# Optimization experiments

Measured on AMD Instinct MI355X. Metric: run time of the kernel, lower is better.

## Reference

```python
import jax, jax.numpy as jnp
import numpy as np

EPS = 1e-08
N = 8192
IN_F = 128
OUT_F = 128


def setup_inputs() -> dict:
    key = jax.random.key(0)
    k1, k2, k3, k4, k5 = jax.random.split(key, 5)
    x = jax.random.normal(k1, (N, IN_F), dtype=jnp.float32)
    adj = jax.random.uniform(k2, (N, N), dtype=jnp.float32)
    noise = jax.random.uniform(k3, (N, N), dtype=jnp.float32)
    # xavier_uniform bound = sqrt(6/(in+out))
    bound = float(np.sqrt(6.0 / (IN_F + OUT_F)))
    weight = jax.random.uniform(k4, (IN_F, OUT_F), dtype=jnp.float32,
                                minval=-bound, maxval=bound)
    learnable_adj = jax.random.uniform(k5, (N, N), dtype=jnp.float32)
    return {"x": x, "adj": adj, "noise": noise, "weight": weight,
            "learnable_adj": learnable_adj}


def reference(x, adj, noise, weight, learnable_adj):
    # noise_adj = adj + learnable_adj + eps * rand_like(adj)
    noise_adj = adj + learnable_adj + EPS * noise
    # add self loops (== + eye(N))
    n = noise_adj.shape[0]
    looped_adj = noise_adj + jnp.eye(n, dtype=noise_adj.dtype)
    # symmetric degree normalization: diag(d^-1/2) @ A @ diag(d^-1/2),
    # expressed as row/col broadcast scaling (same math, O(n^2))
    degree = jnp.sum(looped_adj, axis=1)              # (N,)
    d_inv_sqrt = (degree + EPS) ** -0.5               # (N,)
    normalized_adj = looped_adj * d_inv_sqrt[:, None] * d_inv_sqrt[None, :]
    support = x @ weight                              # (N, out)
    out = normalized_adj @ support                    # (N, out)
    return out
```

## Files before the change

### kernel.cpp

```cpp
#include <hip/hip_runtime.h>
#include <hip/hip_bf16.h>
#include <cstddef>

#define NN 8192
#define FF 128
#define EPSF 1e-8f
#define KSPLIT 8

typedef __attribute__((ext_vector_type(8))) short short8_t;
typedef __attribute__((ext_vector_type(4))) float f32x4_t;

static __device__ __forceinline__ unsigned short f2bf(float f) {
    unsigned u = __builtin_bit_cast(unsigned, f);
    u = (u + 0x7FFFu + ((u >> 16) & 1u)) >> 16;
    return (unsigned short)u;
}
static __device__ __forceinline__ float bf2f(unsigned short h) {
    return __builtin_bit_cast(float, ((unsigned)h) << 16);
}

__global__ __launch_bounds__(256) void fuse_combine_kernel(
    const float* __restrict__ adj, const float* __restrict__ learn,
    unsigned short* __restrict__ Lb, float* __restrict__ degree)
{
    const int row = blockIdx.x >> 1;
    const size_t base = (size_t)row * NN + (blockIdx.x & 1) * 4096
                      + (size_t)threadIdx.x * 8;
    const f32x4_t a0 = __builtin_nontemporal_load((const f32x4_t*)(adj + base));
    const f32x4_t a1 = __builtin_nontemporal_load((const f32x4_t*)(adj + base + 4));
    const f32x4_t a2 = __builtin_nontemporal_load((const f32x4_t*)(adj + base + 2048));
    const f32x4_t a3 = __builtin_nontemporal_load((const f32x4_t*)(adj + base + 2052));
    const f32x4_t l0 = __builtin_nontemporal_load((const f32x4_t*)(learn + base));
    const f32x4_t l1 = __builtin_nontemporal_load((const f32x4_t*)(learn + base + 4));
    const f32x4_t l2 = __builtin_nontemporal_load((const f32x4_t*)(learn + base + 2048));
    const f32x4_t l3 = __builtin_nontemporal_load((const f32x4_t*)(learn + base + 2052));

    const f32x4_t v0 = a0 + l0, v1 = a1 + l1, v2 = a2 + l2, v3 = a3 + l3;
    short8_t p0, p1;
    p0[0] = (short)f2bf(v0.x); p0[1] = (short)f2bf(v0.y);
    p0[2] = (short)f2bf(v0.z); p0[3] = (short)f2bf(v0.w);
    p0[4] = (short)f2bf(v1.x); p0[5] = (short)f2bf(v1.y);
    p0[6] = (short)f2bf(v1.z); p0[7] = (short)f2bf(v1.w);
    p1[0] = (short)f2bf(v2.x); p1[1] = (short)f2bf(v2.y);
    p1[2] = (short)f2bf(v2.z); p1[3] = (short)f2bf(v2.w);
    p1[4] = (short)f2bf(v3.x); p1[5] = (short)f2bf(v3.y);
    p1[6] = (short)f2bf(v3.z); p1[7] = (short)f2bf(v3.w);
    *(short8_t*)(Lb + base) = p0;
    *(short8_t*)(Lb + base + 2048) = p1;

    float acc = (v0.x + v0.y) + (v0.z + v0.w) + (v1.x + v1.y) + (v1.z + v1.w)
              + (v2.x + v2.y) + (v2.z + v2.w) + (v3.x + v3.y) + (v3.z + v3.w);
#pragma unroll
    for (int o = 32; o; o >>= 1) acc += __shfl_down(acc, o);
    __shared__ float red[4];
    if ((threadIdx.x & 63) == 0) red[threadIdx.x >> 6] = acc;
    __syncthreads();
    if (threadIdx.x == 0)
        atomicAdd(degree + row, red[0] + red[1] + red[2] + red[3]);
}

__global__ __launch_bounds__(256) void s_kernel(
    const float* __restrict__ degree, float* __restrict__ s)
{
    const int i = blockIdx.x * 256 + threadIdx.x;
    s[i] = rsqrtf(degree[i] + 1.0f + EPSF);
}

__global__ __launch_bounds__(256) void support_kernel(
    const float* __restrict__ x, const float* __restrict__ w,
    const float* __restrict__ s, unsigned short* __restrict__ ss_t)
{
    __shared__ float Ws[128 * 128];
    __shared__ float Xs[32][128];
    for (int i = threadIdx.x; i < 128 * 128 / 4; i += 256)
        ((float4*)Ws)[i] = ((const float4*)w)[i];
    const int rbase = blockIdx.x * 32;
    for (int i = threadIdx.x; i < 32 * 128 / 4; i += 256)
        ((float4*)&Xs[0][0])[i] = ((const float4*)(x + (size_t)rbase * 128))[i];
    __syncthreads();

    const int c = threadIdx.x & 127;
    const int h = threadIdx.x >> 7;
    for (int r = h; r < 32; r += 2) {
        float acc = 0.f;
#pragma unroll 8
        for (int k = 0; k < 128; ++k) acc += Xs[r][k] * Ws[k * 128 + c];
        const int grow = rbase + r;
        ss_t[(size_t)c * NN + grow] = f2bf(acc * s[grow]);
    }
}

template<bool ATOMIC>
__global__ __launch_bounds__(256) void spmm_bf16_kernel(
    const unsigned short* __restrict__ Lb,
    const unsigned short* __restrict__ ss_t,
    const float* __restrict__ s, float* __restrict__ outp)
{
    const int ks   = blockIdx.y;
    const int i0   = blockIdx.x * 128;
    const int wave = threadIdx.x >> 6;
    const int lane = threadIdx.x & 63;
    const int m = lane & 15;
    const int b = lane >> 4;
    const size_t a0off = (size_t)(i0 + wave * 32 + m) * NN;
    const size_t a1off = a0off + (size_t)16 * NN;
    const int kbeg = ks * (NN / KSPLIT);

    f32x4_t acc[2][8];
#pragma unroll
    for (int f = 0; f < 2; ++f)
#pragma unroll
        for (int t = 0; t < 8; ++t) acc[f][t] = (f32x4_t){0.f, 0.f, 0.f, 0.f};

    for (int kk = kbeg; kk < kbeg + NN / KSPLIT; kk += 32) {
        const int col = kk + 8 * b;
        const short8_t af0 = *(const short8_t*)(Lb + a0off + col);
        const short8_t af1 = *(const short8_t*)(Lb + a1off + col);
#pragma unroll
        for (int nt = 0; nt < 8; ++nt) {
            const short8_t bf =
                *(const short8_t*)(ss_t + (size_t)(nt * 16 + m) * NN + col);
            acc[0][nt] = __builtin_amdgcn_mfma_f32_16x16x32_bf16(af0, bf,
                                                                 acc[0][nt], 0, 0, 0);
            acc[1][nt] = __builtin_amdgcn_mfma_f32_16x16x32_bf16(af1, bf,
                                                                 acc[1][nt], 0, 0, 0);
        }
    }

#pragma unroll
    for (int f = 0; f < 2; ++f) {
#pragma unroll
        for (int nt = 0; nt < 8; ++nt) {
            const int n = nt * 16 + m;
#pragma unroll
            for (int r = 0; r < 4; ++r) {
                const int ro = i0 + wave * 32 + f * 16 + 4 * b + r;
                float v = acc[f][nt][r];
                if (ATOMIC) {
                    if (ks == 0) v += bf2f(ss_t[(size_t)n * NN + ro]);
                    atomicAdd(outp + (size_t)ro * FF + n, s[ro] * v);
                } else {
                    outp[(size_t)ks * NN * FF + (size_t)ro * FF + n] = v;
                }
            }
        }
    }
}

__global__ __launch_bounds__(256) void reduce_kernel(
    const float* __restrict__ part, const unsigned short* __restrict__ ss_t,
    const float* __restrict__ s, float* __restrict__ out)
{
    const int idx = blockIdx.x * 256 + threadIdx.x;
    const int gi = idx >> 7;
    const int cc = idx & 127;
    float v = 0.f;
#pragma unroll
    for (int k = 0; k < KSPLIT; ++k) v += part[(size_t)k * NN * FF + idx];
    v += bf2f(ss_t[(size_t)cc * NN + gi]);
    out[idx] = s[gi] * v;
}

extern "C" void kernel_launch(void* const* d_in, const int* in_sizes, int n_in,
                              void* d_out, int out_size, void* d_ws, size_t ws_size,
                              hipStream_t stream) {
    const float* x     = (const float*)d_in[0];
    const float* adj   = (const float*)d_in[1];
    const float* w     = (const float*)d_in[3];
    const float* learn = (const float*)d_in[4];
    float* out = (float*)d_out;

    float* degree = (float*)d_ws;
    float* s      = degree + NN;
    unsigned short* ss_t = (unsigned short*)(s + NN);
    unsigned short* Lb   = ss_t + (size_t)FF * NN;
    float* part          = (float*)(Lb + (size_t)NN * NN);

    const size_t need_base = 2 * NN * 4 + (size_t)FF * NN * 2
                           + (size_t)NN * NN * 2;
    const size_t need_part = need_base + (size_t)KSPLIT * NN * FF * 4;

    hipMemsetAsync(degree, 0, NN * sizeof(float), stream);
    fuse_combine_kernel<<<NN * 2, 256, 0, stream>>>(adj, learn, Lb, degree);
    s_kernel<<<NN / 256, 256, 0, stream>>>(degree, s);
    support_kernel<<<NN / 32, 256, 0, stream>>>(x, w, s, ss_t);

    if (ws_size >= need_part) {
        spmm_bf16_kernel<false><<<dim3(NN / 128, KSPLIT), 256, 0, stream>>>(
            Lb, ss_t, s, part);
        reduce_kernel<<<NN * FF / 256, 256, 0, stream>>>(part, ss_t, s, out);
    } else {
        hipMemsetAsync(d_out, 0, (size_t)NN * FF * sizeof(float), stream);
        spmm_bf16_kernel<true><<<dim3(NN / 128, KSPLIT), 256, 0, stream>>>(
            Lb, ss_t, s, out);
    }
}
```

Baseline: 258.1 us.

## Pre-swizzle bf16 adjacency and support into MFMA fragment-tiled layouts

The combine kernel now writes the bf16 adjacency in a blocked layout where each 16x32 MFMA A-fragment is contiguous, and the support kernel writes its transposed output in a matching B-fragment-tiled layout. The SpMM kernel then loads each fragment as one contiguous 1 KB chunk per wave instead of 16 rows strided by NN. This is meant to improve coalescing and cache-line use in the main GEMM, at the cost of scattered 16-byte stores in the producer kernels and more complex index math in the reduce epilogue.

Result: slower. 264.6 us (+2.5%).

```diff
diff --git a/kernel.cpp b/kernel.cpp
--- a/kernel.cpp
+++ b/kernel.cpp
@@ -19,13 +19,22 @@
     return __builtin_bit_cast(float, ((unsigned)h) << 16);
 }
 
+static __device__ __forceinline__ size_t lb2_idx(int row, int k) {
+    return ((size_t)(row >> 4) * 256 + (k >> 5)) * 512
+         + ((row & 15) * 4 + ((k >> 3) & 3)) * 8 + (k & 7);
+}
+static __device__ __forceinline__ size_t ss2_idx(int n, int k) {
+    return ((size_t)(k >> 5) * 8 + (n >> 4)) * 512
+         + ((n & 15) * 4 + ((k >> 3) & 3)) * 8 + (k & 7);
+}
+
 __global__ __launch_bounds__(256) void fuse_combine_kernel(
     const float* __restrict__ adj, const float* __restrict__ learn,
     unsigned short* __restrict__ Lb, float* __restrict__ degree)
 {
     const int row = blockIdx.x >> 1;
-    const size_t base = (size_t)row * NN + (blockIdx.x & 1) * 4096
-                      + (size_t)threadIdx.x * 8;
+    const int e0 = (blockIdx.x & 1) * 4096 + threadIdx.x * 8;
+    const size_t base = (size_t)row * NN + e0;
     const f32x4_t a0 = __builtin_nontemporal_load((const f32x4_t*)(adj + base));
     const f32x4_t a1 = __builtin_nontemporal_load((const f32x4_t*)(adj + base + 4));
     const f32x4_t a2 = __builtin_nontemporal_load((const f32x4_t*)(adj + base + 2048));
@@ -45,8 +54,8 @@
     p1[2] = (short)f2bf(v2.z); p1[3] = (short)f2bf(v2.w);
     p1[4] = (short)f2bf(v3.x); p1[5] = (short)f2bf(v3.y);
     p1[6] = (short)f2bf(v3.z); p1[7] = (short)f2bf(v3.w);
-    *(short8_t*)(Lb + base) = p0;
-    *(short8_t*)(Lb + base + 2048) = p1;
+    *(short8_t*)(Lb + lb2_idx(row, e0)) = p0;
+    *(short8_t*)(Lb + lb2_idx(row, e0 + 2048)) = p1;
 
     float acc = (v0.x + v0.y) + (v0.z + v0.w) + (v1.x + v1.y) + (v1.z + v1.w)
               + (v2.x + v2.y) + (v2.z + v2.w) + (v3.x + v3.y) + (v3.z + v3.w);
@@ -68,7 +77,7 @@
 
 __global__ __launch_bounds__(256) void support_kernel(
     const float* __restrict__ x, const float* __restrict__ w,
-    const float* __restrict__ s, unsigned short* __restrict__ ss_t)
+    const float* __restrict__ s, unsigned short* __restrict__ ss2)
 {
     __shared__ float Ws[128 * 128];
     __shared__ float Xs[32][128];
@@ -86,14 +95,14 @@
 #pragma unroll 8
         for (int k = 0; k < 128; ++k) acc += Xs[r][k] * Ws[k * 128 + c];
         const int grow = rbase + r;
-        ss_t[(size_t)c * NN + grow] = f2bf(acc * s[grow]);
+        ss2[ss2_idx(c, grow)] = f2bf(acc * s[grow]);
     }
 }
 
 template<bool ATOMIC>
 __global__ __launch_bounds__(256) void spmm_bf16_kernel(
     const unsigned short* __restrict__ Lb,
-    const unsigned short* __restrict__ ss_t,
+    const unsigned short* __restrict__ ss2,
     const float* __restrict__ s, float* __restrict__ outp)
 {
     const int ks   = blockIdx.y;
@@ -102,9 +111,9 @@
     const int lane = threadIdx.x & 63;
     const int m = lane & 15;
     const int b = lane >> 4;
-    const size_t a0off = (size_t)(i0 + wave * 32 + m) * NN;
-    const size_t a1off = a0off + (size_t)16 * NN;
-    const int kbeg = ks * (NN / KSPLIT);
+    const int laneoff = (m * 4 + b) * 8;
+    const int rb0 = (i0 >> 4) + wave * 2;
+    const int kb0 = ks * (256 / KSPLIT);
 
     f32x4_t acc[2][8];
 #pragma unroll
@@ -112,14 +121,17 @@
 #pragma unroll
         for (int t = 0; t < 8; ++t) acc[f][t] = (f32x4_t){0.f, 0.f, 0.f, 0.f};
 
-    for (int kk = kbeg; kk < kbeg + NN / KSPLIT; kk += 32) {
-        const int col = kk + 8 * b;
-        const short8_t af0 = *(const short8_t*)(Lb + a0off + col);
-        const short8_t af1 = *(const short8_t*)(Lb + a1off + col);
+    const unsigned short* a0p = Lb + (size_t)(rb0 + 0) * 256 * 512 + laneoff;
+    const unsigned short* a1p = Lb + (size_t)(rb0 + 1) * 256 * 512 + laneoff;
+    const unsigned short* bp  = ss2 + laneoff;
+
+    for (int kb = kb0; kb < kb0 + 256 / KSPLIT; ++kb) {
+        const short8_t af0 = *(const short8_t*)(a0p + (size_t)kb * 512);
+        const short8_t af1 = *(const short8_t*)(a1p + (size_t)kb * 512);
 #pragma unroll
         for (int nt = 0; nt < 8; ++nt) {
             const short8_t bf =
-                *(const short8_t*)(ss_t + (size_t)(nt * 16 + m) * NN + col);
+                *(const short8_t*)(bp + (size_t)kb * 4096 + nt * 512);
             acc[0][nt] = __builtin_amdgcn_mfma_f32_16x16x32_bf16(af0, bf,
                                                                  acc[0][nt], 0, 0, 0);
             acc[1][nt] = __builtin_amdgcn_mfma_f32_16x16x32_bf16(af1, bf,
@@ -137,7 +149,7 @@
                 const int ro = i0 + wave * 32 + f * 16 + 4 * b + r;
                 float v = acc[f][nt][r];
                 if (ATOMIC) {
-                    if (ks == 0) v += bf2f(ss_t[(size_t)n * NN + ro]);
+                    if (ks == 0) v += bf2f(ss2[ss2_idx(n, ro)]);
                     atomicAdd(outp + (size_t)ro * FF + n, s[ro] * v);
                 } else {
                     outp[(size_t)ks * NN * FF + (size_t)ro * FF + n] = v;
@@ -148,7 +160,7 @@
 }
 
 __global__ __launch_bounds__(256) void reduce_kernel(
-    const float* __restrict__ part, const unsigned short* __restrict__ ss_t,
+    const float* __restrict__ part, const unsigned short* __restrict__ ss2,
     const float* __restrict__ s, float* __restrict__ out)
 {
     const int idx = blockIdx.x * 256 + threadIdx.x;
@@ -157,7 +169,7 @@
     float v = 0.f;
 #pragma unroll
     for (int k = 0; k < KSPLIT; ++k) v += part[(size_t)k * NN * FF + idx];
-    v += bf2f(ss_t[(size_t)cc * NN + gi]);
+    v += bf2f(ss2[ss2_idx(cc, gi)]);
     out[idx] = s[gi] * v;
 }
 
@@ -172,9 +184,9 @@
 
     float* degree = (float*)d_ws;
     float* s      = degree + NN;
-    unsigned short* ss_t = (unsigned short*)(s + NN);
-    unsigned short* Lb   = ss_t + (size_t)FF * NN;
-    float* part          = (float*)(Lb + (size_t)NN * NN);
+    unsigned short* ss2 = (unsigned short*)(s + NN);
+    unsigned short* Lb  = ss2 + (size_t)FF * NN;
+    float* part         = (float*)(Lb + (size_t)NN * NN);
 
     const size_t need_base = 2 * NN * 4 + (size_t)FF * NN * 2
                            + (size_t)NN * NN * 2;
@@ -183,15 +195,15 @@
     hipMemsetAsync(degree, 0, NN * sizeof(float), stream);
     fuse_combine_kernel<<<NN * 2, 256, 0, stream>>>(adj, learn, Lb, degree);
     s_kernel<<<NN / 256, 256, 0, stream>>>(degree, s);
-    support_kernel<<<NN / 32, 256, 0, stream>>>(x, w, s, ss_t);
+    support_kernel<<<NN / 32, 256, 0, stream>>>(x, w, s, ss2);
 
     if (ws_size >= need_part) {
         spmm_bf16_kernel<false><<<dim3(NN / 128, KSPLIT), 256, 0, stream>>>(
-            Lb, ss_t, s, part);
-        reduce_kernel<<<NN * FF / 256, 256, 0, stream>>>(part, ss_t, s, out);
+            Lb, ss2, s, part);
+        reduce_kernel<<<NN * FF / 256, 256, 0, stream>>>(part, ss2, s, out);
     } else {
         hipMemsetAsync(d_out, 0, (size_t)NN * FF * sizeof(float), stream);
         spmm_bf16_kernel<true><<<dim3(NN / 128, KSPLIT), 256, 0, stream>>>(
-            Lb, ss_t, s, out);
-    }
-}
+            Lb, ss2, s, out);
+    }
+}
```
